# Kernel optimization log

Measured on AMD Instinct MI355X. Metric: run time of the kernel, lower is better.

The kernel has to match this reference:

```python
import jax, jax.numpy as jnp
import numpy as np

B, N, D, H = 2, 2048, 1024, 16
DH = D // H
SCALE = 1.0 / np.sqrt(DH).astype(np.float32)


def setup_inputs() -> dict:
    key = jax.random.key(0)
    k1, k2, k3, k4, k5 = jax.random.split(key, 5)
    x = jax.random.normal(k1, (B, N, D), dtype=jnp.float32)
    attn_bias = jax.random.normal(k2, (B, N, N), dtype=jnp.float32)
    # valid lengths in [N//2, N]; True = keep
    lengths = jax.random.randint(k3, (B,), N // 2, N + 1)
    key_padding_mask = jnp.arange(N)[None, :] < lengths[:, None]
    Wqkv = jax.random.normal(k4, (3 * D, D), dtype=jnp.float32) / np.sqrt(D)
    Wproj = jax.random.normal(k5, (D, D), dtype=jnp.float32) / np.sqrt(D)
    bproj = jnp.zeros((D,), dtype=jnp.float32)
    return {"x": x, "attn_bias": attn_bias, "key_padding_mask": key_padding_mask,
            "Wqkv": Wqkv, "Wproj": Wproj, "bproj": bproj}


def reference(x, attn_bias, key_padding_mask, Wqkv, Wproj, bproj):
    b, n, d = x.shape
    qkv = x @ Wqkv.T                                   # [B,N,3D]
    qkv = qkv.reshape(b, n, 3, H, DH)
    q = jnp.transpose(qkv[:, :, 0], (0, 2, 1, 3))      # [B,H,N,DH]
    k = jnp.transpose(qkv[:, :, 1], (0, 2, 1, 3))
    v = jnp.transpose(qkv[:, :, 2], (0, 2, 1, 3))
    attn = jnp.einsum('bhnd,bhmd->bhnm', q, k) * SCALE  # [B,H,N,N]
    attn = attn + attn_bias[:, None, :, :]
    attn = jnp.where(key_padding_mask[:, None, None, :], attn, -jnp.inf)
    attn = jax.nn.softmax(attn, axis=-1)
    y = jnp.einsum('bhnm,bhmd->bhnd', attn, v)          # [B,H,N,DH]
    y = jnp.transpose(y, (0, 2, 1, 3)).reshape(b, n, d)
    return y @ Wproj.T + bproj
```

## Files before the change

### kernel.cpp

```cpp
#include <hip/hip_runtime.h>
#include <hip/hip_bf16.h>

namespace {

typedef short short8 __attribute__((ext_vector_type(8)));
typedef float f32x4 __attribute__((ext_vector_type(4)));

#define L2E 1.4426950408889634f
#define SB() __builtin_amdgcn_sched_barrier(0)

__device__ __forceinline__ unsigned short f2bf(float f) {
  union { __hip_bfloat16 h; unsigned short u; } cv;
  cv.h = __float2bfloat16(f);
  return cv.u;
}

__device__ __forceinline__ unsigned cvt_pk_bf16(float lo, float hi) {
  unsigned r;
  asm("v_cvt_pk_bf16_f32 %0, %1, %2" : "=v"(r) : "v"(lo), "v"(hi));
  return r;
}

__device__ __forceinline__ void load_lds16(const void* g, void* l) {
  __builtin_amdgcn_global_load_lds((__attribute__((address_space(1))) void*)g,
                                   (__attribute__((address_space(3))) void*)l,
                                   16, 0, 0);
}

__device__ __forceinline__ int pi64(int rho) {
  const int c32 = rho & 32;
  const int o = (rho >> 4) & 1;
  const int g = (rho >> 2) & 3;
  const int s = rho & 3;
  return c32 + (o ? (((g ^ 2) << 3) + 4 + s) : ((g << 3) + s));
}

__global__ __launch_bounds__(256) void cvt_all(const float4* __restrict__ x,
                                               const float4* __restrict__ wqkv,
                                               const float4* __restrict__ wproj,
                                               ushort4* __restrict__ xb,
                                               ushort4* __restrict__ wqkvb,
                                               ushort4* __restrict__ wprojb) {
  int i = blockIdx.x * 256 + threadIdx.x;
  const float4* src;
  ushort4* dst;
  int off;
  if (i < 1048576) { src = x; dst = xb; off = i; }
  else if (i < 1048576 + 786432) { src = wqkv; dst = wqkvb; off = i - 1048576; }
  else { src = wproj; dst = wprojb; off = i - (1048576 + 786432); }
  float4 f = src[off];
  ushort4 u;
  u.x = f2bf(f.x); u.y = f2bf(f.y); u.z = f2bf(f.z); u.w = f2bf(f.w);
  dst[off] = u;
}

__global__ __launch_bounds__(256) void gemm_qkv(const unsigned short* __restrict__ Xb,
                                                const unsigned short* __restrict__ Wb,
                                                unsigned short* __restrict__ qws,
                                                unsigned short* __restrict__ kws,
                                                unsigned short* __restrict__ vTws) {
  __shared__ unsigned short lA[128 * 32];
  __shared__ unsigned short lB[128 * 32];
  const int t = threadIdx.x;
  const int w = t >> 6, l = t & 63;
  const int wm = w >> 1, wn = w & 1;
  const int lr = l & 15, lg = l >> 4;
  const int row0 = blockIdx.x * 128, col0 = blockIdx.y * 128;
  const int srow = t >> 2;
  const int schunk = (t & 3) ^ (srow & 3);
  f32x4 acc[4][4] = {};
  for (int k0 = 0; k0 < 1024; k0 += 32) {
    __syncthreads();
    load_lds16(Xb + (size_t)(row0 + srow) * 1024 + k0 + schunk * 8, &lA[w * 512]);
    load_lds16(Xb + (size_t)(row0 + 64 + srow) * 1024 + k0 + schunk * 8, &lA[2048 + w * 512]);
    load_lds16(Wb + (size_t)(col0 + srow) * 1024 + k0 + schunk * 8, &lB[w * 512]);
    load_lds16(Wb + (size_t)(col0 + 64 + srow) * 1024 + k0 + schunk * 8, &lB[2048 + w * 512]);
    __syncthreads();
    short8 af[4], bf[4];
    const int rslot = (lg ^ (l & 3)) * 8;
#pragma unroll
    for (int mi = 0; mi < 4; ++mi)
      af[mi] = *(const short8*)&lA[(wm * 64 + mi * 16 + lr) * 32 + rslot];
#pragma unroll
    for (int ni = 0; ni < 4; ++ni)
      bf[ni] = *(const short8*)&lB[(wn * 64 + ni * 16 + lr) * 32 + rslot];
#pragma unroll
    for (int mi = 0; mi < 4; ++mi)
#pragma unroll
      for (int ni = 0; ni < 4; ++ni)
        acc[mi][ni] = __builtin_amdgcn_mfma_f32_16x16x32_bf16(af[mi], bf[ni], acc[mi][ni], 0, 0, 0);
  }
#pragma unroll
  for (int mi = 0; mi < 4; ++mi)
#pragma unroll
    for (int ni = 0; ni < 4; ++ni) {
      const int col = col0 + wn * 64 + ni * 16 + lr;
      const int s = col >> 10, rem = col & 1023;
      const int hh = rem >> 6, dh = rem & 63;
      const int row = row0 + wm * 64 + mi * 16 + lg * 4;
      const int bb = row >> 11, n = row & 2047;
      const size_t bh = (size_t)(bb * 16 + hh);
      if (s == 2) {
        ushort4 u4;
        u4.x = f2bf(acc[mi][ni][0]); u4.y = f2bf(acc[mi][ni][1]);
        u4.z = f2bf(acc[mi][ni][2]); u4.w = f2bf(acc[mi][ni][3]);
        *(ushort4*)&vTws[(bh * 64 + dh) * 2048 + n] = u4;
      } else if (s == 0) {
#pragma unroll
        for (int r = 0; r < 4; ++r)
          qws[(bh * 2048 + n + r) * 64 + dh] = f2bf(acc[mi][ni][r] * 0.18033688011112042f);
      } else {
#pragma unroll
        for (int r = 0; r < 4; ++r)
          kws[(bh * 2048 + n + r) * 64 + dh] = f2bf(acc[mi][ni][r]);
      }
    }
}

__global__ __launch_bounds__(256, 4) void attn_fwd(const unsigned short* __restrict__ qws,
                                                   const unsigned short* __restrict__ kws,
                                                   const unsigned short* __restrict__ vTws,
                                                   const float* __restrict__ bias,
                                                   const int* __restrict__ mask,
                                                   unsigned short* __restrict__ ctx) {
  __shared__ unsigned short lK[2][64 * 64];
  __shared__ unsigned short lVT[2][64 * 64];
  __shared__ int lred[4];
  const int t = threadIdx.x, w = t >> 6, l = t & 63;
  const int lr = l & 15, lg = l >> 4;
  const int xr7 = lr & 7;

  const int lin = blockIdx.x;
  const int xcd = lin & 7;
  const int r7 = lin >> 3;
  const int G = xcd * 8 + (r7 & 7);
  const int h = r7 >> 3;
  const int b = G & 1;
  const int qt = G >> 1;

  const size_t bh = (size_t)(b * 16 + h);
  const unsigned short* Q = qws + bh * (2048 * 64);
  const unsigned short* K = kws + bh * (2048 * 64);
  const unsigned short* VT = vTws + bh * (64 * 2048);
  const float* brow = bias + (size_t)b * (2048 * 2048);

  const int* mrow = mask + b * 2048;
  int scnt = 0;
#pragma unroll
  for (int i = 0; i < 8; ++i) scnt += (mrow[t + i * 256] != 0);
#pragma unroll
  for (int d = 1; d < 64; d <<= 1) scnt += __shfl_xor(scnt, d, 64);
  if (l == 0) lred[w] = scnt;
  __syncthreads();
  const int len = lred[0] + lred[1] + lred[2] + lred[3];
  const int nt = ((((len + 63) >> 6) + 1) & ~1);

  const int qv = qt * 64 + w * 16 + lr;
  const short8 qf0 = *(const short8*)&Q[(size_t)qv * 64 + lg * 8];
  const short8 qf1 = *(const short8*)&Q[(size_t)qv * 64 + 32 + lg * 8];
  const float* bq = brow + (size_t)qv * 2048;

  const int be = lg * 8, bo = ((lg ^ 2) * 8) + 4;
  const int boffs[4] = {be, bo, 32 + be, 32 + bo};

  short8 vones;
#pragma unroll
  for (int i = 0; i < 8; ++i) vones[i] = (short)0x3F80;

  f32x4 o[5] = {};

  const int sr = l >> 3;
  const int sc = ((l & 7) ^ sr) * 8;

  auto STAGE = [&](int ti2) {
    const int slot = ti2 & 1;
    const int kt2 = ti2 << 6;
#pragma unroll
    for (int u = 0; u < 2; ++u) {
      const int row = w * 16 + u * 8 + sr;
      load_lds16(K + (size_t)(kt2 + pi64(row)) * 64 + sc, &lK[slot][(w * 16 + u * 8) * 64]);
      load_lds16(VT + (size_t)row * 2048 + kt2 + sc, &lVT[slot][(w * 16 + u * 8) * 64]);
    }
  };
  auto LOADB = [&](float4 (&d)[4], int ti2) {
    const int kt2 = ti2 << 6;
#pragma unroll
    for (int j = 0; j < 4; ++j) d[j] = *(const float4*)&bq[kt2 + boffs[j]];
  };
  auto COMPUTE = [&](int ti, float4 (&b4)[4], bool hn2) {
    const int slot = ti & 1;
    const int kt = ti << 6;
    const unsigned short* lKs = lK[slot];
    const unsigned short* lVs = lVT[slot];
    f32x4 s4[4];
    __builtin_amdgcn_s_setprio(1);
#pragma unroll
    for (int j = 0; j < 4; ++j) {
      f32x4 sj = {-16.f, -16.f, -16.f, -16.f};
      const int krow = (j * 16 + lr) * 64;
      short8 kf0 = *(const short8*)&lKs[krow + (lg ^ xr7) * 8];
      short8 kf1 = *(const short8*)&lKs[krow + ((lg + 4) ^ xr7) * 8];
      sj = __builtin_amdgcn_mfma_f32_16x16x32_bf16(kf0, qf0, sj, 0, 0, 0);
      sj = __builtin_amdgcn_mfma_f32_16x16x32_bf16(kf1, qf1, sj, 0, 0, 0);
      s4[j] = sj;
    }
    __builtin_amdgcn_s_setprio(0);
    if (kt + 64 <= len) {
#pragma unroll
      for (int j = 0; j < 4; ++j) {
        s4[j][0] = fmaf(b4[j].x, L2E, s4[j][0]);
        s4[j][1] = fmaf(b4[j].y, L2E, s4[j][1]);
        s4[j][2] = fmaf(b4[j].z, L2E, s4[j][2]);
        s4[j][3] = fmaf(b4[j].w, L2E, s4[j][3]);
      }
    } else {
#pragma unroll
      for (int j = 0; j < 4; ++j) {
        const int kb = kt + boffs[j];
        const float* bp = &b4[j].x;
#pragma unroll
        for (int r = 0; r < 4; ++r)
          s4[j][r] = (kb + r < len) ? fmaf(bp[r], L2E, s4[j][r]) : -1e30f;
      }
    }
    if (hn2) LOADB(b4, ti + 2);
#pragma unroll
    for (int j = 0; j < 4; ++j)
#pragma unroll
      for (int r = 0; r < 4; ++r) s4[j][r] = exp2f(s4[j][r]);
    unsigned wj0[4], wj1[4];
#pragma unroll
    for (int j = 0; j < 4; ++j) {
      wj0[j] = cvt_pk_bf16(s4[j][0], s4[j][1]);
      wj1[j] = cvt_pk_bf16(s4[j][2], s4[j][3]);
    }
#pragma unroll
    for (int c = 0; c < 2; ++c) {
      union { unsigned u[4]; short8 s8; } pu;
      pu.u[0] = wj0[2 * c];
      pu.u[1] = wj1[2 * c];
      pu.u[2] = (unsigned)__shfl_xor((int)wj0[2 * c + 1], 32, 64);
      pu.u[3] = (unsigned)__shfl_xor((int)wj1[2 * c + 1], 32, 64);
      __builtin_amdgcn_s_setprio(1);
#pragma unroll
      for (int ni = 0; ni < 4; ++ni) {
        short8 vf = *(const short8*)&lVs[(ni * 16 + lr) * 64 + ((c * 4 + lg) ^ xr7) * 8];
        o[ni] = __builtin_amdgcn_mfma_f32_16x16x32_bf16(pu.s8, vf, o[ni], 0, 0, 0);
      }
      o[4] = __builtin_amdgcn_mfma_f32_16x16x32_bf16(pu.s8, vones, o[4], 0, 0, 0);
      __builtin_amdgcn_s_setprio(0);
    }
  };

  float4 bA[4], bB[4];
  SB();
  STAGE(0);
  SB();
  LOADB(bA, 0);
  LOADB(bB, 1);
  SB();
  asm volatile("s_waitcnt vmcnt(4)" ::: "memory");
  __builtin_amdgcn_s_barrier();
  SB();

  for (int ti = 0; ti < nt; ti += 2) {
    const bool h2 = (ti + 2 < nt);
    SB();
    STAGE(ti + 1);
    SB();
    COMPUTE(ti, bA, h2);
    SB();
    asm volatile("s_waitcnt vmcnt(4) lgkmcnt(0)" ::: "memory");
    __builtin_amdgcn_s_barrier();
    SB();
    if (h2) { STAGE(ti + 2); SB(); }
    COMPUTE(ti + 1, bB, h2);
    if (h2) {
      SB();
      asm volatile("s_waitcnt vmcnt(4) lgkmcnt(0)" ::: "memory");
      __builtin_amdgcn_s_barrier();
      SB();
    }
  }

  float linv[4];
#pragma unroll
  for (int r = 0; r < 4; ++r) linv[r] = 1.0f / o[4][r];
#pragma unroll
  for (int r = 0; r < 4; ++r) {
    const size_t orow = (size_t)b * 2048 + qt * 64 + w * 16 + lg * 4 + r;
#pragma unroll
    for (int ni = 0; ni < 4; ++ni)
      ctx[orow * 1024 + h * 64 + ni * 16 + lr] = f2bf(o[ni][r] * linv[r]);
  }
}

__global__ __launch_bounds__(256) void gemm_proj(const unsigned short* __restrict__ Cb,
                                                 const unsigned short* __restrict__ Wb,
                                                 const float* __restrict__ bproj,
                                                 float* __restrict__ out) {
  __shared__ unsigned short lA[128 * 32];
  __shared__ unsigned short lB[128 * 32];
  const int t = threadIdx.x;
  const int w = t >> 6, l = t & 63;
  const int wm = w >> 1, wn = w & 1;
  const int lr = l & 15, lg = l >> 4;
  const int row0 = blockIdx.x * 128, col0 = blockIdx.y * 128;
  const int srow = t >> 2;
  const int schunk = (t & 3) ^ (srow & 3);
  f32x4 acc[4][4] = {};
  for (int k0 = 0; k0 < 1024; k0 += 32) {
    __syncthreads();
    load_lds16(Cb + (size_t)(row0 + srow) * 1024 + k0 + schunk * 8, &lA[w * 512]);
    load_lds16(Cb + (size_t)(row0 + 64 + srow) * 1024 + k0 + schunk * 8, &lA[2048 + w * 512]);
    load_lds16(Wb + (size_t)(col0 + srow) * 1024 + k0 + schunk * 8, &lB[w * 512]);
    load_lds16(Wb + (size_t)(col0 + 64 + srow) * 1024 + k0 + schunk * 8, &lB[2048 + w * 512]);
    __syncthreads();
    short8 af[4], bf[4];
    const int rslot = (lg ^ (l & 3)) * 8;
#pragma unroll
    for (int mi = 0; mi < 4; ++mi)
      af[mi] = *(const short8*)&lA[(wm * 64 + mi * 16 + lr) * 32 + rslot];
#pragma unroll
    for (int ni = 0; ni < 4; ++ni)
      bf[ni] = *(const short8*)&lB[(wn * 64 + ni * 16 + lr) * 32 + rslot];
#pragma unroll
    for (int mi = 0; mi < 4; ++mi)
#pragma unroll
      for (int ni = 0; ni < 4; ++ni)
        acc[mi][ni] = __builtin_amdgcn_mfma_f32_16x16x32_bf16(af[mi], bf[ni], acc[mi][ni], 0, 0, 0);
  }
#pragma unroll
  for (int mi = 0; mi < 4; ++mi)
#pragma unroll
    for (int ni = 0; ni < 4; ++ni) {
      const int col = col0 + wn * 64 + ni * 16 + lr;
      const float bp = bproj[col];
#pragma unroll
      for (int r = 0; r < 4; ++r) {
        const int row = row0 + wm * 64 + mi * 16 + lg * 4 + r;
        out[(size_t)row * 1024 + col] = acc[mi][ni][r] + bp;
      }
    }
}

}

extern "C" void kernel_launch(void* const* d_in, const int* in_sizes, int n_in,
                              void* d_out, int out_size, void* d_ws, size_t ws_size,
                              hipStream_t stream) {
  (void)in_sizes; (void)n_in; (void)out_size; (void)ws_size;
  const float* x        = (const float*)d_in[0];
  const float* attnbias = (const float*)d_in[1];
  const int*   mask     = (const int*)d_in[2];
  const float* Wqkv     = (const float*)d_in[3];
  const float* Wproj    = (const float*)d_in[4];
  const float* bproj    = (const float*)d_in[5];
  float* out = (float*)d_out;

  unsigned short* ws     = (unsigned short*)d_ws;
  unsigned short* xb     = ws;
  unsigned short* wqkvb  = xb + 4194304;
  unsigned short* wprojb = wqkvb + 3145728;
  unsigned short* qws    = wprojb + 1048576;
  unsigned short* kws    = qws + 4194304;
  unsigned short* vTws   = kws + 4194304;
  unsigned short* ctxb   = vTws + 4194304;

  cvt_all<<<8192, 256, 0, stream>>>((const float4*)x, (const float4*)Wqkv,
                                    (const float4*)Wproj, (ushort4*)xb,
                                    (ushort4*)wqkvb, (ushort4*)wprojb);
  gemm_qkv<<<dim3(32, 24), 256, 0, stream>>>(xb, wqkvb, qws, kws, vTws);
  attn_fwd<<<1024, 256, 0, stream>>>(qws, kws, vTws, attnbias, mask, ctxb);
  gemm_proj<<<dim3(32, 8), 256, 0, stream>>>(ctxb, wprojb, bproj, out);
}
```

Baseline: 150.3 us.

## Process two query groups per wave in attention with 128-thread blocks

The attention kernel now runs 2 waves per block instead of 4, and each wave handles 32 query rows (two 16-row groups) instead of 16. Each K and V fragment read from LDS is therefore reused for two MFMA groups, which halves LDS reads per unit of compute. Staging loops and wait counts are widened to match. The mask length is now reduced within a single wave, removing the cross-wave LDS reduction and barrier, and exp2f and the reciprocal use hardware intrinsics. The cost is more registers per wave and fewer waves to hide latency, since the launch-bounds occupancy hint is also dropped.

```diff
diff --git a/kernel.cpp b/kernel.cpp
--- a/kernel.cpp
+++ b/kernel.cpp
@@ -117,15 +117,14 @@
     }
 }
 
-__global__ __launch_bounds__(256, 4) void attn_fwd(const unsigned short* __restrict__ qws,
-                                                   const unsigned short* __restrict__ kws,
-                                                   const unsigned short* __restrict__ vTws,
-                                                   const float* __restrict__ bias,
-                                                   const int* __restrict__ mask,
-                                                   unsigned short* __restrict__ ctx) {
+__global__ __launch_bounds__(128) void attn_fwd(const unsigned short* __restrict__ qws,
+                                                const unsigned short* __restrict__ kws,
+                                                const unsigned short* __restrict__ vTws,
+                                                const float* __restrict__ bias,
+                                                const int* __restrict__ mask,
+                                                unsigned short* __restrict__ ctx) {
   __shared__ unsigned short lK[2][64 * 64];
   __shared__ unsigned short lVT[2][64 * 64];
-  __shared__ int lred[4];
   const int t = threadIdx.x, w = t >> 6, l = t & 63;
   const int lr = l & 15, lg = l >> 4;
   const int xr7 = lr & 7;
@@ -142,23 +141,28 @@
   const unsigned short* Q = qws + bh * (2048 * 64);
   const unsigned short* K = kws + bh * (2048 * 64);
   const unsigned short* VT = vTws + bh * (64 * 2048);
-  const float* brow = bias + (size_t)b * (2048 * 2048);
-
-  const int* mrow = mask + b * 2048;
+
+  const int4* m4 = (const int4*)(mask + b * 2048);
   int scnt = 0;
 #pragma unroll
-  for (int i = 0; i < 8; ++i) scnt += (mrow[t + i * 256] != 0);
+  for (int i = 0; i < 8; ++i) {
+    int4 v = m4[l + i * 64];
+    scnt += (v.x != 0) + (v.y != 0) + (v.z != 0) + (v.w != 0);
+  }
 #pragma unroll
   for (int d = 1; d < 64; d <<= 1) scnt += __shfl_xor(scnt, d, 64);
-  if (l == 0) lred[w] = scnt;
-  __syncthreads();
-  const int len = lred[0] + lred[1] + lred[2] + lred[3];
+  const int len = scnt;
   const int nt = ((((len + 63) >> 6) + 1) & ~1);
 
-  const int qv = qt * 64 + w * 16 + lr;
-  const short8 qf0 = *(const short8*)&Q[(size_t)qv * 64 + lg * 8];
-  const short8 qf1 = *(const short8*)&Q[(size_t)qv * 64 + 32 + lg * 8];
-  const float* bq = brow + (size_t)qv * 2048;
+  short8 qf[2][2];
+  const float* bq[2];
+#pragma unroll
+  for (int qg = 0; qg < 2; ++qg) {
+    const int qv = qt * 64 + w * 32 + qg * 16 + lr;
+    qf[qg][0] = *(const short8*)&Q[(size_t)qv * 64 + lg * 8];
+    qf[qg][1] = *(const short8*)&Q[(size_t)qv * 64 + 32 + lg * 8];
+    bq[qg] = bias + (size_t)b * (2048 * 2048) + (size_t)qv * 2048;
+  }
 
   const int be = lg * 8, bo = ((lg ^ 2) * 8) + 4;
   const int boffs[4] = {be, bo, 32 + be, 32 + bo};
@@ -167,7 +171,8 @@
 #pragma unroll
   for (int i = 0; i < 8; ++i) vones[i] = (short)0x3F80;
 
-  f32x4 o[5] = {};
+  f32x4 o0[5] = {};
+  f32x4 o1[5] = {};
 
   const int sr = l >> 3;
   const int sc = ((l & 7) ^ sr) * 8;
@@ -176,90 +181,109 @@
     const int slot = ti2 & 1;
     const int kt2 = ti2 << 6;
 #pragma unroll
-    for (int u = 0; u < 2; ++u) {
-      const int row = w * 16 + u * 8 + sr;
-      load_lds16(K + (size_t)(kt2 + pi64(row)) * 64 + sc, &lK[slot][(w * 16 + u * 8) * 64]);
-      load_lds16(VT + (size_t)row * 2048 + kt2 + sc, &lVT[slot][(w * 16 + u * 8) * 64]);
+    for (int u = 0; u < 4; ++u) {
+      const int row = w * 32 + u * 8 + sr;
+      load_lds16(K + (size_t)(kt2 + pi64(row)) * 64 + sc, &lK[slot][(w * 32 + u * 8) * 64]);
+      load_lds16(VT + (size_t)row * 2048 + kt2 + sc, &lVT[slot][(w * 32 + u * 8) * 64]);
     }
   };
-  auto LOADB = [&](float4 (&d)[4], int ti2) {
+  auto LOADB = [&](float4 (&d)[2][4], int ti2) {
     const int kt2 = ti2 << 6;
 #pragma unroll
-    for (int j = 0; j < 4; ++j) d[j] = *(const float4*)&bq[kt2 + boffs[j]];
+    for (int qg = 0; qg < 2; ++qg)
+#pragma unroll
+      for (int j = 0; j < 4; ++j) d[qg][j] = *(const float4*)&bq[qg][kt2 + boffs[j]];
   };
-  auto COMPUTE = [&](int ti, float4 (&b4)[4], bool hn2) {
+  auto COMPUTE = [&](int ti, float4 (&b4)[2][4], bool hn2) {
     const int slot = ti & 1;
     const int kt = ti << 6;
     const unsigned short* lKs = lK[slot];
     const unsigned short* lVs = lVT[slot];
-    f32x4 s4[4];
+    f32x4 s4[2][4];
     __builtin_amdgcn_s_setprio(1);
 #pragma unroll
     for (int j = 0; j < 4; ++j) {
-      f32x4 sj = {-16.f, -16.f, -16.f, -16.f};
       const int krow = (j * 16 + lr) * 64;
       short8 kf0 = *(const short8*)&lKs[krow + (lg ^ xr7) * 8];
       short8 kf1 = *(const short8*)&lKs[krow + ((lg + 4) ^ xr7) * 8];
-      sj = __builtin_amdgcn_mfma_f32_16x16x32_bf16(kf0, qf0, sj, 0, 0, 0);
-      sj = __builtin_amdgcn_mfma_f32_16x16x32_bf16(kf1, qf1, sj, 0, 0, 0);
-      s4[j] = sj;
+#pragma unroll
+      for (int qg = 0; qg < 2; ++qg) {
+        f32x4 sj = {-16.f, -16.f, -16.f, -16.f};
+        sj = __builtin_amdgcn_mfma_f32_16x16x32_bf16(kf0, qf[qg][0], sj, 0, 0, 0);
+        sj = __builtin_amdgcn_mfma_f32_16x16x32_bf16(kf1, qf[qg][1], sj, 0, 0, 0);
+        s4[qg][j] = sj;
+      }
     }
     __builtin_amdgcn_s_setprio(0);
     if (kt + 64 <= len) {
 #pragma unroll
+      for (int qg = 0; qg < 2; ++qg)
+#pragma unroll
+        for (int j = 0; j < 4; ++j) {
+          s4[qg][j][0] = fmaf(b4[qg][j].x, L2E, s4[qg][j][0]);
+          s4[qg][j][1] = fmaf(b4[qg][j].y, L2E, s4[qg][j][1]);
+          s4[qg][j][2] = fmaf(b4[qg][j].z, L2E, s4[qg][j][2]);
+          s4[qg][j][3] = fmaf(b4[qg][j].w, L2E, s4[qg][j][3]);
+        }
+    } else {
+#pragma unroll
+      for (int qg = 0; qg < 2; ++qg)
+#pragma unroll
+        for (int j = 0; j < 4; ++j) {
+          const int kb = kt + boffs[j];
+          const float* bp = &b4[qg][j].x;
+#pragma unroll
+          for (int r = 0; r < 4; ++r)
+            s4[qg][j][r] = (kb + r < len) ? fmaf(bp[r], L2E, s4[qg][j][r]) : -1e30f;
+        }
+    }
+    if (hn2) LOADB(b4, ti + 2);
+#pragma unroll
+    for (int qg = 0; qg < 2; ++qg)
+#pragma unroll
+      for (int j = 0; j < 4; ++j)
+#pragma unroll
+        for (int r = 0; r < 4; ++r) s4[qg][j][r] = __builtin_amdgcn_exp2f(s4[qg][j][r]);
+    unsigned wj0[2][4], wj1[2][4];
+#pragma unroll
+    for (int qg = 0; qg < 2; ++qg)
+#pragma unroll
       for (int j = 0; j < 4; ++j) {
-        s4[j][0] = fmaf(b4[j].x, L2E, s4[j][0]);
-        s4[j][1] = fmaf(b4[j].y, L2E, s4[j][1]);
-        s4[j][2] = fmaf(b4[j].z, L2E, s4[j][2]);
-        s4[j][3] = fmaf(b4[j].w, L2E, s4[j][3]);
+        wj0[qg][j] = cvt_pk_bf16(s4[qg][j][0], s4[qg][j][1]);
+        wj1[qg][j] = cvt_pk_bf16(s4[qg][j][2], s4[qg][j][3]);
       }
-    } else {
-#pragma unroll
-      for (int j = 0; j < 4; ++j) {
-        const int kb = kt + boffs[j];
-        const float* bp = &b4[j].x;
-#pragma unroll
-        for (int r = 0; r < 4; ++r)
-          s4[j][r] = (kb + r < len) ? fmaf(bp[r], L2E, s4[j][r]) : -1e30f;
-      }
-    }
-    if (hn2) LOADB(b4, ti + 2);
-#pragma unroll
-    for (int j = 0; j < 4; ++j)
-#pragma unroll
-      for (int r = 0; r < 4; ++r) s4[j][r] = exp2f(s4[j][r]);
-    unsigned wj0[4], wj1[4];
-#pragma unroll
-    for (int j = 0; j < 4; ++j) {
-      wj0[j] = cvt_pk_bf16(s4[j][0], s4[j][1]);
-      wj1[j] = cvt_pk_bf16(s4[j][2], s4[j][3]);
-    }
 #pragma unroll
     for (int c = 0; c < 2; ++c) {
-      union { unsigned u[4]; short8 s8; } pu;
-      pu.u[0] = wj0[2 * c];
-      pu.u[1] = wj1[2 * c];
-      pu.u[2] = (unsigned)__shfl_xor((int)wj0[2 * c + 1], 32, 64);
-      pu.u[3] = (unsigned)__shfl_xor((int)wj1[2 * c + 1], 32, 64);
+      union { unsigned u[4]; short8 s8; } pu0, pu1;
+      pu0.u[0] = wj0[0][2 * c];
+      pu0.u[1] = wj1[0][2 * c];
+      pu0.u[2] = (unsigned)__shfl_xor((int)wj0[0][2 * c + 1], 32, 64);
+      pu0.u[3] = (unsigned)__shfl_xor((int)wj1[0][2 * c + 1], 32, 64);
+      pu1.u[0] = wj0[1][2 * c];
+      pu1.u[1] = wj1[1][2 * c];
+      pu1.u[2] = (unsigned)__shfl_xor((int)wj0[1][2 * c + 1], 32, 64);
+      pu1.u[3] = (unsigned)__shfl_xor((int)wj1[1][2 * c + 1], 32, 64);
       __builtin_amdgcn_s_setprio(1);
 #pragma unroll
       for (int ni = 0; ni < 4; ++ni) {
         short8 vf = *(const short8*)&lVs[(ni * 16 + lr) * 64 + ((c * 4 + lg) ^ xr7) * 8];
-        o[ni] = __builtin_amdgcn_mfma_f32_16x16x32_bf16(pu.s8, vf, o[ni], 0, 0, 0);
+        o0[ni] = __builtin_amdgcn_mfma_f32_16x16x32_bf16(pu0.s8, vf, o0[ni], 0, 0, 0);
+        o1[ni] = __builtin_amdgcn_mfma_f32_16x16x32_bf16(pu1.s8, vf, o1[ni], 0, 0, 0);
       }
-      o[4] = __builtin_amdgcn_mfma_f32_16x16x32_bf16(pu.s8, vones, o[4], 0, 0, 0);
+      o0[4] = __builtin_amdgcn_mfma_f32_16x16x32_bf16(pu0.s8, vones, o0[4], 0, 0, 0);
+      o1[4] = __builtin_amdgcn_mfma_f32_16x16x32_bf16(pu1.s8, vones, o1[4], 0, 0, 0);
       __builtin_amdgcn_s_setprio(0);
     }
   };
 
-  float4 bA[4], bB[4];
+  float4 bA[2][4], bB[2][4];
   SB();
   STAGE(0);
   SB();
   LOADB(bA, 0);
   LOADB(bB, 1);
   SB();
-  asm volatile("s_waitcnt vmcnt(4)" ::: "memory");
+  asm volatile("s_waitcnt vmcnt(8)" ::: "memory");
   __builtin_amdgcn_s_barrier();
   SB();
 
@@ -270,28 +294,30 @@
     SB();
     COMPUTE(ti, bA, h2);
     SB();
-    asm volatile("s_waitcnt vmcnt(4) lgkmcnt(0)" ::: "memory");
+    asm volatile("s_waitcnt vmcnt(8) lgkmcnt(0)" ::: "memory");
     __builtin_amdgcn_s_barrier();
     SB();
     if (h2) { STAGE(ti + 2); SB(); }
     COMPUTE(ti + 1, bB, h2);
     if (h2) {
       SB();
-      asm volatile("s_waitcnt vmcnt(4) lgkmcnt(0)" ::: "memory");
+      asm volatile("s_waitcnt vmcnt(8) lgkmcnt(0)" ::: "memory");
       __builtin_amdgcn_s_barrier();
       SB();
     }
   }
 
-  float linv[4];
-#pragma unroll
-  for (int r = 0; r < 4; ++r) linv[r] = 1.0f / o[4][r];
 #pragma unroll
   for (int r = 0; r < 4; ++r) {
-    const size_t orow = (size_t)b * 2048 + qt * 64 + w * 16 + lg * 4 + r;
-#pragma unroll
-    for (int ni = 0; ni < 4; ++ni)
-      ctx[orow * 1024 + h * 64 + ni * 16 + lr] = f2bf(o[ni][r] * linv[r]);
+    const float li0 = __builtin_amdgcn_rcpf(o0[4][r]);
+    const float li1 = __builtin_amdgcn_rcpf(o1[4][r]);
+    const size_t or0 = (size_t)b * 2048 + qt * 64 + w * 32 + lg * 4 + r;
+    const size_t or1 = or0 + 16;
+#pragma unroll
+    for (int ni = 0; ni < 4; ++ni) {
+      ctx[or0 * 1024 + h * 64 + ni * 16 + lr] = f2bf(o0[ni][r] * li0);
+      ctx[or1 * 1024 + h * 64 + ni * 16 + lr] = f2bf(o1[ni][r] * li1);
+    }
   }
 }
 
@@ -371,6 +397,6 @@
                                     (const float4*)Wproj, (ushort4*)xb,
                                     (ushort4*)wqkvb, (ushort4*)wprojb);
   gemm_qkv<<<dim3(32, 24), 256, 0, stream>>>(xb, wqkvb, qws, kws, vTws);
-  attn_fwd<<<1024, 256, 0, stream>>>(qws, kws, vTws, attnbias, mask, ctxb);
+  attn_fwd<<<1024, 128, 0, stream>>>(qws, kws, vTws, attnbias, mask, ctxb);
   gemm_proj<<<dim3(32, 8), 256, 0, stream>>>(ctxb, wprojb, bproj, out);
 }
```

Measured after the change: 162.9 us. 8.3% more time.
